# Kernel tuning notes

Measured on AMD Instinct MI355X. Metric: run time of the kernel, lower is better.

## Reference

```python
import jax, jax.numpy as jnp
import numpy as np
from jax import lax

N_SAMPLES = 2 ** 15      # 32768
D_SIZE = 256             # number of dictionary atoms
KERNEL = 256             # atom length
N_STEPS = 16             # sparse_coding_iterations
CHANNELS = 128


def setup_inputs() -> dict:
    key = jax.random.key(0)
    ks = jax.random.split(key, 9)
    B = 8
    x = jax.random.normal(ks[0], (B, N_SAMPLES), dtype=jnp.float32)
    # dictionary, initialized uniform(-1, 1) as in nn.Parameter(...).uniform_(-1, 1)
    d = jax.random.uniform(ks[1], (D_SIZE, KERNEL), dtype=jnp.float32, minval=-1.0, maxval=1.0)
    # 1x1 Conv1d weights stored as (out, in); biases (out,)
    w_pos_amp = jax.random.normal(ks[2], (CHANNELS, 2), dtype=jnp.float32) * 0.1
    b_pos_amp = jnp.zeros((CHANNELS,), dtype=jnp.float32)
    w_atoms = jax.random.normal(ks[3], (CHANNELS, D_SIZE), dtype=jnp.float32) * 0.05
    b_atoms = jnp.zeros((CHANNELS,), dtype=jnp.float32)
    w_reduce = jax.random.normal(ks[4], (CHANNELS, 2 * CHANNELS), dtype=jnp.float32) * 0.05
    b_reduce = jnp.zeros((CHANNELS,), dtype=jnp.float32)
    return {
        'x': x, 'd': d,
        'w_pos_amp': w_pos_amp, 'b_pos_amp': b_pos_amp,
        'w_atoms': w_atoms, 'b_atoms': b_atoms,
        'w_reduce': w_reduce, 'b_reduce': b_reduce,
    }


def _correlate(residual, d):
    # residual: (B, 1, N), d: (D, K) -> feature map (B, D, N-K+1) (valid cross-correlation,
    # identical to torch F.conv1d with no padding)
    return lax.conv_general_dilated(
        residual, d[:, None, :], window_strides=(1,), padding='VALID',
        dimension_numbers=('NCH', 'OIH', 'NCH'))


def _matching_pursuit(x3, d):
    """16-step greedy matching pursuit. Returns key points (B, 2+D, N_STEPS) and residual."""
    B = x3.shape[0]
    T = N_SAMPLES - KERNEL + 1  # valid correlation length

    def step(residual, _):
        fm = _correlate(residual, d)                       # (B, D, T)
        flat = fm.reshape(B, -1)
        idx = jnp.argmax(jnp.abs(flat), axis=1)            # best (atom, pos) per example
        amp = jnp.take_along_axis(flat, idx[:, None], axis=1)[:, 0]
        atom_idx = idx // T
        pos = idx % T

        def subtract(r, p, ai, a):
            seg = lax.dynamic_slice(r, (p,), (KERNEL,))
            return lax.dynamic_update_slice(r, seg - a * d[ai], (p,))

        new_res = jax.vmap(subtract)(residual[:, 0, :], pos, atom_idx, amp)[:, None, :]
        enc = jnp.concatenate([
            (pos.astype(jnp.float32) / T)[:, None],        # normalized position
            amp[:, None],                                  # amplitude
            jax.nn.one_hot(atom_idx, D_SIZE, dtype=jnp.float32),  # atom one-hot
        ], axis=1)                                         # (B, 2+D)
        return new_res, enc

    residual, encs = lax.scan(step, x3, None, length=N_STEPS)  # encs: (S, B, 2+D)
    kp = jnp.transpose(encs, (1, 2, 0))                        # (B, 2+D, S)
    return kp, residual


def _conv1x1(w, b, x):
    # w: (O, C), x: (B, C, T) -> (B, O, T)
    return jnp.einsum('oc,bct->bot', w, x) + b[None, :, None]


def reference(x, d, w_pos_amp, b_pos_amp, w_atoms, b_atoms, w_reduce, b_reduce):
    B = x.shape[0]
    x3 = x.reshape(B, 1, N_SAMPLES)
    kp, _ = _matching_pursuit(x3, d)          # (B, 258, 16)
    pos_amp = kp[:, :2, :]
    atoms = kp[:, 2:, :]
    pa = _conv1x1(w_pos_amp, b_pos_amp, pos_amp)
    at = _conv1x1(w_atoms, b_atoms, atoms)
    h = jnp.concatenate([pa, at], axis=1)     # (B, 2*channels, 16)
    return _conv1x1(w_reduce, b_reduce, h)    # (B, channels, 16)
```

## Files before the change

### kernel.cpp

```cpp
#include <hip/hip_runtime.h>
#include <hip/hip_bf16.h>
#include <float.h>

#define NS 32768
#define KER 256
#define TOUT 32513
#define NATOM 256
#define NSTEP 16
#define BATCH 8
#define NBLK 255
#define XSTR 33024
#define SW4(i) ((i) + (((i) >> 5) << 2))

typedef __attribute__((ext_vector_type(8))) _Float16 half8;
typedef __attribute__((ext_vector_type(16))) float f32x16;
typedef __attribute__((ext_vector_type(4))) unsigned int uint4v;

__device__ __forceinline__ void cmax(float& ba, float& bs, float& bi,
                                     float oa, float os, float oi) {
    if (oa > ba || (oa == ba && oi < bi)) { ba = oa; bs = os; bi = oi; }
}

__device__ __forceinline__ void fma8(float acc[8], float4 dA, float4 dB,
                                     float4 w0, float4 w1, float4 w2, float4 w3) {
    float w[16] = {w0.x,w0.y,w0.z,w0.w, w1.x,w1.y,w1.z,w1.w,
                   w2.x,w2.y,w2.z,w2.w, w3.x,w3.y,w3.z,w3.w};
    float dv[8] = {dA.x,dA.y,dA.z,dA.w, dB.x,dB.y,dB.z,dB.w};
#pragma unroll
    for (int i = 0; i < 8; ++i)
#pragma unroll
        for (int j = 0; j < 8; ++j)
            acc[j] = fmaf(dv[i], w[i + j], acc[j]);
}

__device__ __forceinline__ unsigned short f16hi(float v) {
    return __builtin_bit_cast(unsigned short, (_Float16)v);
}
__device__ __forceinline__ unsigned short f16lo(float v) {
    const _Float16 h = (_Float16)v;
    return __builtin_bit_cast(unsigned short, (_Float16)(v - (float)h));
}

__global__ __launch_bounds__(256) void k_prep(const float* __restrict__ x,
                                              const float* __restrict__ d,
                                              uint4* __restrict__ xhl4,
                                              uint4* __restrict__ dhF,
                                              uint4* __restrict__ dlF) {
    const int gid = blockIdx.x * 256 + threadIdx.x;
    const int NXE = BATCH * XSTR;
    if (gid < NXE) {
        const int b = gid / XSTR, i = gid - b * XSTR;
        float v[4];
#pragma unroll
        for (int u = 0; u < 4; ++u)
            v[u] = (i + u < NS) ? x[b * NS + i + u] : 0.f;
        uint4 q;
        q.x = (unsigned int)f16hi(v[0]) | ((unsigned int)f16hi(v[1]) << 16);
        q.y = (unsigned int)f16hi(v[2]) | ((unsigned int)f16hi(v[3]) << 16);
        q.z = (unsigned int)f16lo(v[0]) | ((unsigned int)f16lo(v[1]) << 16);
        q.w = (unsigned int)f16lo(v[2]) | ((unsigned int)f16lo(v[3]) << 16);
        xhl4[gid] = q;
    } else {
        const int j = gid - NXE;
        if (j < NATOM * 32) {
            const int kg = j >> 8, atom = j & 255;
            const float* dp = d + atom * 256 + (kg << 3);
            uint4 hw, lw;
            hw.x = (unsigned int)f16hi(dp[0]) | ((unsigned int)f16hi(dp[1]) << 16);
            hw.y = (unsigned int)f16hi(dp[2]) | ((unsigned int)f16hi(dp[3]) << 16);
            hw.z = (unsigned int)f16hi(dp[4]) | ((unsigned int)f16hi(dp[5]) << 16);
            hw.w = (unsigned int)f16hi(dp[6]) | ((unsigned int)f16hi(dp[7]) << 16);
            lw.x = (unsigned int)f16lo(dp[0]) | ((unsigned int)f16lo(dp[1]) << 16);
            lw.y = (unsigned int)f16lo(dp[2]) | ((unsigned int)f16lo(dp[3]) << 16);
            lw.z = (unsigned int)f16lo(dp[4]) | ((unsigned int)f16lo(dp[5]) << 16);
            lw.w = (unsigned int)f16lo(dp[6]) | ((unsigned int)f16lo(dp[7]) << 16);
            dhF[(kg << 8) + atom] = hw;
            dlF[(kg << 8) + atom] = lw;
        }
    }
}

__global__ __launch_bounds__(256) void k_init(const uint4* __restrict__ xhl4,
                                              const uint4* __restrict__ dhF,
                                              const uint4* __restrict__ dlF,
                                              float2* __restrict__ bm) {
    const int c = blockIdx.x, mg = blockIdx.y, b = blockIdx.z;
    const int tid = threadIdx.x;
    const int w = tid >> 6, l = tid & 63;
    const int n = l & 31, h = l >> 5;
    __shared__ uint4 xw[512];
    __shared__ unsigned long long wmax[4][64];
    const int t0 = c << 8;
    xw[tid] = xhl4[b * XSTR + t0 + tid];
    xw[tid + 256] = xhl4[b * XSTR + t0 + 256 + tid];
    __syncthreads();

    f32x16 acc00, acc01, acc10, acc11;
#pragma unroll
    for (int j = 0; j < 16; ++j) { acc00[j] = 0.f; acc01[j] = 0.f;
                                   acc10[j] = 0.f; acc11[j] = 0.f; }

    const int abase = (mg << 6) + n;
    const int sbb = (w << 6) + n + (h << 3);

    half8 fbh[4], fbl[4];
    {
        const uint4 q0 = xw[sbb], q1 = xw[sbb + 4];
        const uint4v hv = {q0.x, q0.y, q1.x, q1.y};
        const uint4v lv = {q0.z, q0.w, q1.z, q1.w};
        fbh[0] = __builtin_bit_cast(half8, hv);
        fbl[0] = __builtin_bit_cast(half8, lv);
    }
    {
        const uint4 q0 = xw[sbb + 16], q1 = xw[sbb + 20];
        const uint4v hv = {q0.x, q0.y, q1.x, q1.y};
        const uint4v lv = {q0.z, q0.w, q1.z, q1.w};
        fbh[1] = __builtin_bit_cast(half8, hv);
        fbl[1] = __builtin_bit_cast(half8, lv);
    }

#pragma unroll 4
    for (int kk = 0; kk < 16; ++kk) {
        const int kg = (kk << 1) + h;
        const half8 ah0 = __builtin_bit_cast(half8, dhF[(kg << 8) + abase]);
        const half8 al0 = __builtin_bit_cast(half8, dlF[(kg << 8) + abase]);
        const half8 ah1 = __builtin_bit_cast(half8, dhF[(kg << 8) + abase + 32]);
        const half8 al1 = __builtin_bit_cast(half8, dlF[(kg << 8) + abase + 32]);
        {
            const int sN = sbb + ((kk + 2) << 4);
            const uint4 q0 = xw[sN], q1 = xw[sN + 4];
            const uint4v hv = {q0.x, q0.y, q1.x, q1.y};
            const uint4v lv = {q0.z, q0.w, q1.z, q1.w};
            fbh[(kk + 2) & 3] = __builtin_bit_cast(half8, hv);
            fbl[(kk + 2) & 3] = __builtin_bit_cast(half8, lv);
        }
        const half8 b0h = fbh[kk & 3],       b0l = fbl[kk & 3];
        const half8 b1h = fbh[(kk + 2) & 3], b1l = fbl[(kk + 2) & 3];
        acc00 = __builtin_amdgcn_mfma_f32_32x32x16_f16(ah0, b0l, acc00, 0, 0, 0);
        acc00 = __builtin_amdgcn_mfma_f32_32x32x16_f16(al0, b0h, acc00, 0, 0, 0);
        acc00 = __builtin_amdgcn_mfma_f32_32x32x16_f16(ah0, b0h, acc00, 0, 0, 0);
        acc10 = __builtin_amdgcn_mfma_f32_32x32x16_f16(ah1, b0l, acc10, 0, 0, 0);
        acc10 = __builtin_amdgcn_mfma_f32_32x32x16_f16(al1, b0h, acc10, 0, 0, 0);
        acc10 = __builtin_amdgcn_mfma_f32_32x32x16_f16(ah1, b0h, acc10, 0, 0, 0);
        acc01 = __builtin_amdgcn_mfma_f32_32x32x16_f16(ah0, b1l, acc01, 0, 0, 0);
        acc01 = __builtin_amdgcn_mfma_f32_32x32x16_f16(al0, b1h, acc01, 0, 0, 0);
        acc01 = __builtin_amdgcn_mfma_f32_32x32x16_f16(ah0, b1h, acc01, 0, 0, 0);
        acc11 = __builtin_amdgcn_mfma_f32_32x32x16_f16(ah1, b1l, acc11, 0, 0, 0);
        acc11 = __builtin_amdgcn_mfma_f32_32x32x16_f16(al1, b1h, acc11, 0, 0, 0);
        acc11 = __builtin_amdgcn_mfma_f32_32x32x16_f16(ah1, b1h, acc11, 0, 0, 0);
    }

    const int tb = t0 + (w << 6) + n;
#pragma unroll
    for (int mt = 0; mt < 2; ++mt) {
#pragma unroll
        for (int r = 0; r < 16; ++r) {
            const int amt = (mt << 5) + (r & 3) + ((r >> 2) << 3) + (h << 2);
            const int idx0 = ((mg << 6) + amt) * TOUT + tb;
            const float v0 = (mt == 0) ? acc00[r] : acc10[r];
            const float v1 = (mt == 0) ? acc01[r] : acc11[r];
            const unsigned int c0 = (0x7FFFFFu - (unsigned int)idx0);
            unsigned long long k0 = 0ull, k1 = 0ull;
            if (tb < TOUT)
                k0 = ((unsigned long long)__float_as_uint(fabsf(v0)) << 32)
                   | ((unsigned long long)(c0 << 1))
                   | (unsigned long long)(__float_as_uint(v0) >> 31);
            if (tb + 32 < TOUT)
                k1 = ((unsigned long long)__float_as_uint(fabsf(v1)) << 32)
                   | ((unsigned long long)((c0 - 32u) << 1))
                   | (unsigned long long)(__float_as_uint(v1) >> 31);
            unsigned long long k = (k1 > k0) ? k1 : k0;
#pragma unroll
            for (int m = 1; m <= 16; m <<= 1) {
                const unsigned long long ok = __shfl_xor(k, m, 32);
                if (ok > k) k = ok;
            }
            if (n == 0) wmax[w][amt] = k;
        }
    }
    __syncthreads();
    if (tid < 128) {
        const int a = tid & 63, p = tid >> 6;
        unsigned long long k = wmax[(p << 1)][a];
        const unsigned long long k2 = wmax[(p << 1) + 1][a];
        if (k2 > k) k = k2;
        const int blk = (c << 1) + p;
        if (blk < NBLK) {
            const float av = __uint_as_float((unsigned int)(k >> 32));
            const unsigned int lo = (unsigned int)k;
            const int idx = 0x7FFFFF - (int)((lo >> 1) & 0x7FFFFFu);
            const float bsg = (lo & 1u) ? -av : av;
            bm[(size_t)((b << 8) + (mg << 6) + a) * NBLK + blk] =
                make_float2(bsg, (float)idx);
        }
    }
}

__global__ __launch_bounds__(256) void k_lvl2(const float2* __restrict__ bm,
                                              float4* __restrict__ l2) {
    const int b = blockIdx.y;
    const int oglob = blockIdx.x * 8 + (threadIdx.x >> 5);
    const int lane = threadIdx.x & 31;
    const float2* row = bm + (size_t)(b * NATOM + oglob) * NBLK;
    float ba = -1.f, bsg = 0.f, bi = 3.0e7f;
    for (int i = lane; i < NBLK; i += 32) {
        const float2 e = row[i];
        cmax(ba, bsg, bi, fabsf(e.x), e.x, e.y);
    }
#pragma unroll
    for (int m = 16; m >= 1; m >>= 1) {
        const float oa = __shfl_xor(ba, m, 32);
        const float os = __shfl_xor(bsg, m, 32);
        const float oi = __shfl_xor(bi, m, 32);
        cmax(ba, bsg, bi, oa, os, oi);
    }
    if (lane == 0) l2[(b << 8) + oglob] = make_float4(ba, bsg, bi, 0.f);
}

__global__ __launch_bounds__(512) void k_step(const float* __restrict__ d,
                                              const float* __restrict__ resid_src,
                                              float* __restrict__ resid_dst,
                                              float2* __restrict__ bm,
                                              float4* __restrict__ l2,
                                              int* __restrict__ pos_a,
                                              int* __restrict__ atom_a,
                                              float* __restrict__ amp_a,
                                              int step) {
    const int og = blockIdx.x, b = blockIdx.y;
    const int tid = threadIdx.x;
    const int wave = tid >> 6, lane = tid & 63;
    __shared__ float dt[2048];
    __shared__ float rsu[1024];
    __shared__ float4 sred[8];
    __shared__ float4 upd[8][5];
    __shared__ int sh_pos, sh_atom, sh_prev;
    __shared__ float sh_amp;

    ((float4*)dt)[tid] = ((const float4*)(d + og * 2048))[tid];
    if (tid == 0 && step >= 2) sh_prev = pos_a[(step - 1) * BATCH + b];
    const float4* l2r = l2 + (step & 1) * (BATCH * NATOM);
    float4*       l2w = l2 + ((step + 1) & 1) * (BATCH * NATOM);

    {
        float ba = -1.f, bsg = 0.f, bi = 3.0e7f;
        if (tid < 256) {
            const float4 e = l2r[(b << 8) + tid];
            ba = e.x; bsg = e.y; bi = e.z;
        }
#pragma unroll
        for (int m = 32; m >= 1; m >>= 1) {
            const float oa = __shfl_xor(ba, m);
            const float os = __shfl_xor(bsg, m);
            const float oi = __shfl_xor(bi, m);
            cmax(ba, bsg, bi, oa, os, oi);
        }
        if (lane == 0) sred[wave] = make_float4(ba, bsg, bi, 0.f);
    }
    __syncthreads();
    if (tid == 0) {
        float4 r = sred[0];
#pragma unroll
        for (int i = 1; i < 8; ++i) {
            const float4 q = sred[i];
            if (q.x > r.x || (q.x == r.x && q.z < r.z)) r = q;
        }
        const int idx = (int)r.z;
        const int atom = idx / TOUT;
        const int pos = idx - atom * TOUT;
        sh_pos = pos; sh_atom = atom; sh_amp = r.y;
        if (og == 0) {
            pos_a[step * BATCH + b] = pos;
            atom_a[step * BATCH + b] = atom;
            amp_a[step * BATCH + b] = r.y;
        }
    }
    __syncthreads();
    const int p = sh_pos, atom_s = sh_atom;
    const float amp = sh_amp;

    if (step < 2) {
        for (int i = tid; i < 1024; i += 512) {
            const int g = (og << 10) + i;
            float v = resid_src[(size_t)b * NS + g];
            const int off = g - p;
            if (off >= 0 && off < KER)
                v = __fsub_rn(v, __fmul_rn(amp, d[atom_s * KER + off]));
            resid_dst[(size_t)b * NS + g] = v;
        }
    } else if (og == 0) {
        if (tid < 256) {
            const int g = p + tid;
            resid_dst[(size_t)b * NS + g] =
                __fsub_rn(resid_src[(size_t)b * NS + g],
                          __fmul_rn(amp, d[atom_s * KER + tid]));
        } else {
            const int g = sh_prev + (tid - 256);
            if (g < p || g > p + 255)
                resid_dst[(size_t)b * NS + g] = resid_src[(size_t)b * NS + g];
        }
    }

    int tlo = p - 255; if (tlo < 0) tlo = 0;
    int thi = p + 255; if (thi > TOUT - 1) thi = TOUT - 1;
    const int bs0 = tlo >> 7, be0 = thi >> 7;
    const int rbase = bs0 << 7;
    const int nblks = be0 - bs0 + 1;
    const int rlen = (nblks << 7) + 255;
    for (int i = tid; i < rlen; i += 512) {
        const int g = rbase + i;
        float v = (g < NS) ? resid_src[(size_t)b * NS + g] : 0.f;
        const int off = g - p;
        if (g < NS && off >= 0 && off < KER)
            v = __fsub_rn(v, __fmul_rn(amp, d[atom_s * KER + off]));
        rsu[SW4(i)] = v;
    }
    __syncthreads();

    const int lg = lane >> 4, l16 = lane & 15;
    const float* dp = dt + (wave << 8) + (lg << 6);
    const int atomg = (og << 3) + wave;
    for (int bb = 0; bb < nblks; ++bb) {
        const int blk = bs0 + bb;
        const int t0r = (bb << 7) + (l16 << 3) + (lg << 6);
        float acc[8];
#pragma unroll
        for (int j = 0; j < 8; ++j) acc[j] = 0.f;
        float4 A0 = *(const float4*)(rsu + SW4(t0r));
        float4 A1 = *(const float4*)(rsu + SW4(t0r + 4));
        float4 B0 = *(const float4*)(rsu + SW4(t0r + 8));
        float4 B1 = *(const float4*)(rsu + SW4(t0r + 12));
#pragma unroll
        for (int kk = 0; kk < 64; kk += 16) {
            const float4 d0 = *(const float4*)(dp + kk);
            const float4 d1 = *(const float4*)(dp + kk + 4);
            const float4 N0 = *(const float4*)(rsu + SW4(t0r + kk + 16));
            const float4 N1 = *(const float4*)(rsu + SW4(t0r + kk + 20));
            fma8(acc, d0, d1, A0, A1, B0, B1);
            const float4 d2 = *(const float4*)(dp + kk + 8);
            const float4 d3 = *(const float4*)(dp + kk + 12);
            const float4 M0 = *(const float4*)(rsu + SW4(t0r + kk + 24));
            const float4 M1 = *(const float4*)(rsu + SW4(t0r + kk + 28));
            fma8(acc, d2, d3, B0, B1, N0, N1);
            A0 = N0; A1 = N1; B0 = M0; B1 = M1;
        }
#pragma unroll
        for (int j = 0; j < 8; ++j) {
            acc[j] += __shfl_xor(acc[j], 16);
            acc[j] += __shfl_xor(acc[j], 32);
        }
        float ba = -1.f, bsg = 0.f, bi = 3.0e7f;
        const int tbp = rbase + (bb << 7) + (l16 << 3);
#pragma unroll
        for (int j = 0; j < 8; ++j) {
            const int t = tbp + j;
            const float av = fabsf(acc[j]);
            if (t < TOUT && av > ba) { ba = av; bsg = acc[j]; bi = (float)(atomg * TOUT + t); }
        }
#pragma unroll
        for (int m = 32; m >= 1; m >>= 1) {
            const float oa = __shfl_xor(ba, m);
            const float os = __shfl_xor(bsg, m);
            const float oi = __shfl_xor(bi, m);
            cmax(ba, bsg, bi, oa, os, oi);
        }
        if (lane == 0) {
            bm[(size_t)(b * NATOM + atomg) * NBLK + blk] = make_float2(bsg, bi);
            upd[wave][bb] = make_float4(ba, bsg, bi, 0.f);
        }
    }
    __syncthreads();

    {
        const float4 eo = l2r[(b << 8) + atomg];
        const int oblk = ((int)eo.z - atomg * TOUT) >> 7;
        if (oblk >= bs0 && oblk <= be0) {
            float ba = -1.f, bsg = 0.f, bi = 3.0e7f;
            const float2* row = bm + (size_t)(b * NATOM + atomg) * NBLK;
            for (int i = lane; i < NBLK; i += 64) {
                if (i >= bs0 && i <= be0) {
                    const float4 e2 = upd[wave][i - bs0];
                    cmax(ba, bsg, bi, e2.x, e2.y, e2.z);
                } else {
                    const float2 e2 = row[i];
                    cmax(ba, bsg, bi, fabsf(e2.x), e2.x, e2.y);
                }
            }
#pragma unroll
            for (int m = 32; m >= 1; m >>= 1) {
                const float oa = __shfl_xor(ba, m);
                const float os = __shfl_xor(bsg, m);
                const float oi = __shfl_xor(bi, m);
                cmax(ba, bsg, bi, oa, os, oi);
            }
            if (lane == 0) l2w[(b << 8) + atomg] = make_float4(ba, bsg, bi, 0.f);
        } else if (lane == 0) {
            float ba = eo.x, bsg = eo.y, bi = eo.z;
            for (int bb = 0; bb < nblks; ++bb) {
                const float4 e2 = upd[wave][bb];
                cmax(ba, bsg, bi, e2.x, e2.y, e2.z);
            }
            l2w[(b << 8) + atomg] = make_float4(ba, bsg, bi, 0.f);
        }
    }
}

__global__ __launch_bounds__(128) void k_head(const int* __restrict__ pos_a,
                                              const int* __restrict__ atom_a,
                                              const float* __restrict__ amp_a,
                                              const float4* __restrict__ l2,
                                              const float* __restrict__ wpa,
                                              const float* __restrict__ bpa,
                                              const float* __restrict__ wat,
                                              const float* __restrict__ bat,
                                              const float* __restrict__ wr,
                                              const float* __restrict__ br,
                                              float* __restrict__ out) {
    const int s = blockIdx.x, b = blockIdx.y;
    const int o = threadIdx.x;
    __shared__ float4 hred[2];
    __shared__ int sh_pos, sh_atom;
    __shared__ float sh_amp;
    int pos, atom; float amp;
    if (s == NSTEP - 1) {
        const float4* l2r = l2 + ((NSTEP - 1) & 1) * (BATCH * NATOM);
        float ba = -1.f, bsg = 0.f, bi = 3.0e7f;
        const float4 e0 = l2r[(b << 8) + o];
        const float4 e1 = l2r[(b << 8) + 128 + o];
        cmax(ba, bsg, bi, e0.x, e0.y, e0.z);
        cmax(ba, bsg, bi, e1.x, e1.y, e1.z);
#pragma unroll
        for (int m = 32; m >= 1; m >>= 1) {
            const float oa = __shfl_xor(ba, m);
            const float os = __shfl_xor(bsg, m);
            const float oi = __shfl_xor(bi, m);
            cmax(ba, bsg, bi, oa, os, oi);
        }
        if ((o & 63) == 0) hred[o >> 6] = make_float4(ba, bsg, bi, 0.f);
        __syncthreads();
        if (o == 0) {
            float4 r = hred[0];
            const float4 q = hred[1];
            if (q.x > r.x || (q.x == r.x && q.z < r.z)) r = q;
            const int idx = (int)r.z;
            sh_atom = idx / TOUT;
            sh_pos = idx - sh_atom * TOUT;
            sh_amp = r.y;
        }
        __syncthreads();
        pos = sh_pos; atom = sh_atom; amp = sh_amp;
    } else {
        pos  = pos_a[s * BATCH + b];
        atom = atom_a[s * BATCH + b];
        amp  = amp_a[s * BATCH + b];
    }
    const float posn = (float)pos / 32513.0f;
    float sum = br[o];
    for (int c = 0; c < 128; ++c) {
        const float pa = wpa[c * 2] * posn + wpa[c * 2 + 1] * amp + bpa[c];
        const float at = wat[c * 256 + atom] + bat[c];
        sum += wr[o * 256 + c] * pa + wr[o * 256 + 128 + c] * at;
    }
    out[(b * 128 + o) * NSTEP + s] = sum;
}

extern "C" void kernel_launch(void* const* d_in, const int* in_sizes, int n_in,
                              void* d_out, int out_size, void* d_ws, size_t ws_size,
                              hipStream_t stream) {
    const float* x   = (const float*)d_in[0];
    const float* d   = (const float*)d_in[1];
    const float* wpa = (const float*)d_in[2];
    const float* bpa = (const float*)d_in[3];
    const float* wat = (const float*)d_in[4];
    const float* bat = (const float*)d_in[5];
    const float* wr  = (const float*)d_in[6];
    const float* br  = (const float*)d_in[7];
    float* out = (float*)d_out;

    char* ws = (char*)d_ws;
    float2* bm     = (float2*)ws;
    float4* l2     = (float4*)(ws + 4177920);
    int*    pos_a  = (int*)(ws + 4243456);
    int*    atom_a = (int*)(ws + 4243968);
    float*  amp_a  = (float*)(ws + 4244480);
    uint4*  dhF    = (uint4*)(ws + 4244992);
    uint4*  dlF    = (uint4*)(ws + 4376064);
    uint4*  xhl4   = (uint4*)(ws + 4507136);
    float*  resid0 = (float*)(ws + 4507136);
    float*  resid1 = (float*)(ws + 5555712);

    const int prep_n = BATCH * XSTR + NATOM * 32;
    k_prep<<<(prep_n + 255) / 256, 256, 0, stream>>>(x, d, xhl4, dhF, dlF);
    k_init<<<dim3(128, 4, 8), 256, 0, stream>>>(xhl4, dhF, dlF, bm);
    k_lvl2<<<dim3(32, 8), 256, 0, stream>>>(bm, l2);
    for (int st = 0; st < NSTEP - 1; ++st) {
        const float* rs = (st == 0) ? x : ((st & 1) ? resid1 : resid0);
        float* rd = (st & 1) ? resid0 : resid1;
        k_step<<<dim3(32, 8), 512, 0, stream>>>(d, rs, rd, bm, l2,
                                                pos_a, atom_a, amp_a, st);
    }
    k_head<<<dim3(16, 8), 128, 0, stream>>>(pos_a, atom_a, amp_a, l2,
                                            wpa, bpa, wat, bat, wr, br, out);
}
```

Measured before the change: 406.2 us.

## Fuse level-2 reduction into init via 64-bit atomicMax keys; halve init atom tile

Drops the separate k_lvl2 kernel. k_init now atomically max-reduces packed 64-bit (abs value, index, sign) keys straight into a per-atom level-2 array, and the step and head kernels use the same packed-key comparison instead of float4 triplets. k_init's atom tile shrinks from 64 to 32 per block, doubling the grid and halving accumulator registers, which may help occupancy but re-reads the x tile twice as often. It also adds a memset launch and global atomics in exchange for removing one kernel launch and the bm re-read.

New measurement: 407.5 us. About the same (+0.3%).

```diff
diff --git a/kernel.cpp b/kernel.cpp
--- a/kernel.cpp
+++ b/kernel.cpp
@@ -15,10 +15,23 @@
 typedef __attribute__((ext_vector_type(8))) _Float16 half8;
 typedef __attribute__((ext_vector_type(16))) float f32x16;
 typedef __attribute__((ext_vector_type(4))) unsigned int uint4v;
+typedef unsigned long long u64;
 
 __device__ __forceinline__ void cmax(float& ba, float& bs, float& bi,
                                      float oa, float os, float oi) {
     if (oa > ba || (oa == ba && oi < bi)) { ba = oa; bs = os; bi = oi; }
+}
+
+__device__ __forceinline__ u64 packkey(float sig, int idx) {
+    return ((u64)__float_as_uint(fabsf(sig)) << 32)
+         | ((u64)((0x7FFFFFu - (unsigned int)idx) << 1))
+         | (u64)(__float_as_uint(sig) >> 31);
+}
+__device__ __forceinline__ void unpackkey(u64 k, float& sig, int& idx) {
+    const float av = __uint_as_float((unsigned int)(k >> 32));
+    const unsigned int lo = (unsigned int)k;
+    idx = 0x7FFFFF - (int)((lo >> 1) & 0x7FFFFFu);
+    sig = (lo & 1u) ? -av : av;
 }
 
 __device__ __forceinline__ void fma8(float acc[8], float4 dA, float4 dB,
@@ -83,24 +96,24 @@
 __global__ __launch_bounds__(256) void k_init(const uint4* __restrict__ xhl4,
                                               const uint4* __restrict__ dhF,
                                               const uint4* __restrict__ dlF,
-                                              float2* __restrict__ bm) {
+                                              float2* __restrict__ bm,
+                                              u64* __restrict__ l2k) {
     const int c = blockIdx.x, mg = blockIdx.y, b = blockIdx.z;
     const int tid = threadIdx.x;
     const int w = tid >> 6, l = tid & 63;
     const int n = l & 31, h = l >> 5;
     __shared__ uint4 xw[512];
-    __shared__ unsigned long long wmax[4][64];
+    __shared__ u64 wmax[4][32];
     const int t0 = c << 8;
     xw[tid] = xhl4[b * XSTR + t0 + tid];
     xw[tid + 256] = xhl4[b * XSTR + t0 + 256 + tid];
     __syncthreads();
 
-    f32x16 acc00, acc01, acc10, acc11;
-#pragma unroll
-    for (int j = 0; j < 16; ++j) { acc00[j] = 0.f; acc01[j] = 0.f;
-                                   acc10[j] = 0.f; acc11[j] = 0.f; }
-
-    const int abase = (mg << 6) + n;
+    f32x16 acc00, acc01;
+#pragma unroll
+    for (int j = 0; j < 16; ++j) { acc00[j] = 0.f; acc01[j] = 0.f; }
+
+    const int abase = (mg << 5) + n;
     const int sbb = (w << 6) + n + (h << 3);
 
     half8 fbh[4], fbl[4];
@@ -124,8 +137,6 @@
         const int kg = (kk << 1) + h;
         const half8 ah0 = __builtin_bit_cast(half8, dhF[(kg << 8) + abase]);
         const half8 al0 = __builtin_bit_cast(half8, dlF[(kg << 8) + abase]);
-        const half8 ah1 = __builtin_bit_cast(half8, dhF[(kg << 8) + abase + 32]);
-        const half8 al1 = __builtin_bit_cast(half8, dlF[(kg << 8) + abase + 32]);
         {
             const int sN = sbb + ((kk + 2) << 4);
             const uint4 q0 = xw[sN], q1 = xw[sN + 4];
@@ -139,89 +150,58 @@
         acc00 = __builtin_amdgcn_mfma_f32_32x32x16_f16(ah0, b0l, acc00, 0, 0, 0);
         acc00 = __builtin_amdgcn_mfma_f32_32x32x16_f16(al0, b0h, acc00, 0, 0, 0);
         acc00 = __builtin_amdgcn_mfma_f32_32x32x16_f16(ah0, b0h, acc00, 0, 0, 0);
-        acc10 = __builtin_amdgcn_mfma_f32_32x32x16_f16(ah1, b0l, acc10, 0, 0, 0);
-        acc10 = __builtin_amdgcn_mfma_f32_32x32x16_f16(al1, b0h, acc10, 0, 0, 0);
-        acc10 = __builtin_amdgcn_mfma_f32_32x32x16_f16(ah1, b0h, acc10, 0, 0, 0);
         acc01 = __builtin_amdgcn_mfma_f32_32x32x16_f16(ah0, b1l, acc01, 0, 0, 0);
         acc01 = __builtin_amdgcn_mfma_f32_32x32x16_f16(al0, b1h, acc01, 0, 0, 0);
         acc01 = __builtin_amdgcn_mfma_f32_32x32x16_f16(ah0, b1h, acc01, 0, 0, 0);
-        acc11 = __builtin_amdgcn_mfma_f32_32x32x16_f16(ah1, b1l, acc11, 0, 0, 0);
-        acc11 = __builtin_amdgcn_mfma_f32_32x32x16_f16(al1, b1h, acc11, 0, 0, 0);
-        acc11 = __builtin_amdgcn_mfma_f32_32x32x16_f16(ah1, b1h, acc11, 0, 0, 0);
     }
 
     const int tb = t0 + (w << 6) + n;
 #pragma unroll
-    for (int mt = 0; mt < 2; ++mt) {
-#pragma unroll
-        for (int r = 0; r < 16; ++r) {
-            const int amt = (mt << 5) + (r & 3) + ((r >> 2) << 3) + (h << 2);
-            const int idx0 = ((mg << 6) + amt) * TOUT + tb;
-            const float v0 = (mt == 0) ? acc00[r] : acc10[r];
-            const float v1 = (mt == 0) ? acc01[r] : acc11[r];
-            const unsigned int c0 = (0x7FFFFFu - (unsigned int)idx0);
-            unsigned long long k0 = 0ull, k1 = 0ull;
-            if (tb < TOUT)
-                k0 = ((unsigned long long)__float_as_uint(fabsf(v0)) << 32)
-                   | ((unsigned long long)(c0 << 1))
-                   | (unsigned long long)(__float_as_uint(v0) >> 31);
-            if (tb + 32 < TOUT)
-                k1 = ((unsigned long long)__float_as_uint(fabsf(v1)) << 32)
-                   | ((unsigned long long)((c0 - 32u) << 1))
-                   | (unsigned long long)(__float_as_uint(v1) >> 31);
-            unsigned long long k = (k1 > k0) ? k1 : k0;
-#pragma unroll
-            for (int m = 1; m <= 16; m <<= 1) {
-                const unsigned long long ok = __shfl_xor(k, m, 32);
-                if (ok > k) k = ok;
-            }
-            if (n == 0) wmax[w][amt] = k;
-        }
-    }
-    __syncthreads();
-    if (tid < 128) {
-        const int a = tid & 63, p = tid >> 6;
-        unsigned long long k = wmax[(p << 1)][a];
-        const unsigned long long k2 = wmax[(p << 1) + 1][a];
+    for (int r = 0; r < 16; ++r) {
+        const int amt = (r & 3) + ((r >> 2) << 3) + (h << 2);
+        const int idx0 = ((mg << 5) + amt) * TOUT + tb;
+        const float v0 = acc00[r], v1 = acc01[r];
+        const unsigned int c0 = (0x7FFFFFu - (unsigned int)idx0);
+        u64 k0 = 0ull, k1 = 0ull;
+        if (tb < TOUT)
+            k0 = ((u64)__float_as_uint(fabsf(v0)) << 32)
+               | ((u64)(c0 << 1))
+               | (u64)(__float_as_uint(v0) >> 31);
+        if (tb + 32 < TOUT)
+            k1 = ((u64)__float_as_uint(fabsf(v1)) << 32)
+               | ((u64)((c0 - 32u) << 1))
+               | (u64)(__float_as_uint(v1) >> 31);
+        u64 k = (k1 > k0) ? k1 : k0;
+#pragma unroll
+        for (int m = 1; m <= 16; m <<= 1) {
+            const u64 ok = __shfl_xor(k, m, 32);
+            if (ok > k) k = ok;
+        }
+        if (n == 0) wmax[w][amt] = k;
+    }
+    __syncthreads();
+    if (tid < 64) {
+        const int a = tid & 31, p = tid >> 5;
+        u64 k = wmax[(p << 1)][a];
+        const u64 k2 = wmax[(p << 1) + 1][a];
         if (k2 > k) k = k2;
         const int blk = (c << 1) + p;
+        const int atom = (mg << 5) + a;
         if (blk < NBLK) {
-            const float av = __uint_as_float((unsigned int)(k >> 32));
-            const unsigned int lo = (unsigned int)k;
-            const int idx = 0x7FFFFF - (int)((lo >> 1) & 0x7FFFFFu);
-            const float bsg = (lo & 1u) ? -av : av;
-            bm[(size_t)((b << 8) + (mg << 6) + a) * NBLK + blk] =
+            float bsg; int idx;
+            unpackkey(k, bsg, idx);
+            bm[(size_t)((b << 8) + atom) * NBLK + blk] =
                 make_float2(bsg, (float)idx);
-        }
-    }
-}
-
-__global__ __launch_bounds__(256) void k_lvl2(const float2* __restrict__ bm,
-                                              float4* __restrict__ l2) {
-    const int b = blockIdx.y;
-    const int oglob = blockIdx.x * 8 + (threadIdx.x >> 5);
-    const int lane = threadIdx.x & 31;
-    const float2* row = bm + (size_t)(b * NATOM + oglob) * NBLK;
-    float ba = -1.f, bsg = 0.f, bi = 3.0e7f;
-    for (int i = lane; i < NBLK; i += 32) {
-        const float2 e = row[i];
-        cmax(ba, bsg, bi, fabsf(e.x), e.x, e.y);
-    }
-#pragma unroll
-    for (int m = 16; m >= 1; m >>= 1) {
-        const float oa = __shfl_xor(ba, m, 32);
-        const float os = __shfl_xor(bsg, m, 32);
-        const float oi = __shfl_xor(bi, m, 32);
-        cmax(ba, bsg, bi, oa, os, oi);
-    }
-    if (lane == 0) l2[(b << 8) + oglob] = make_float4(ba, bsg, bi, 0.f);
+            atomicMax(&l2k[(b << 8) + atom], k);
+        }
+    }
 }
 
 __global__ __launch_bounds__(512) void k_step(const float* __restrict__ d,
                                               const float* __restrict__ resid_src,
                                               float* __restrict__ resid_dst,
                                               float2* __restrict__ bm,
-                                              float4* __restrict__ l2,
+                                              u64* __restrict__ l2,
                                               int* __restrict__ pos_a,
                                               int* __restrict__ atom_a,
                                               float* __restrict__ amp_a,
@@ -231,47 +211,40 @@
     const int wave = tid >> 6, lane = tid & 63;
     __shared__ float dt[2048];
     __shared__ float rsu[1024];
-    __shared__ float4 sred[8];
+    __shared__ u64 sred[8];
     __shared__ float4 upd[8][5];
     __shared__ int sh_pos, sh_atom, sh_prev;
     __shared__ float sh_amp;
 
     ((float4*)dt)[tid] = ((const float4*)(d + og * 2048))[tid];
     if (tid == 0 && step >= 2) sh_prev = pos_a[(step - 1) * BATCH + b];
-    const float4* l2r = l2 + (step & 1) * (BATCH * NATOM);
-    float4*       l2w = l2 + ((step + 1) & 1) * (BATCH * NATOM);
+    u64* l2r = l2 + (step & 1) * (BATCH * NATOM);
+    u64* l2w = l2 + ((step + 1) & 1) * (BATCH * NATOM);
 
     {
-        float ba = -1.f, bsg = 0.f, bi = 3.0e7f;
-        if (tid < 256) {
-            const float4 e = l2r[(b << 8) + tid];
-            ba = e.x; bsg = e.y; bi = e.z;
-        }
-#pragma unroll
-        for (int m = 32; m >= 1; m >>= 1) {
-            const float oa = __shfl_xor(ba, m);
-            const float os = __shfl_xor(bsg, m);
-            const float oi = __shfl_xor(bi, m);
-            cmax(ba, bsg, bi, oa, os, oi);
-        }
-        if (lane == 0) sred[wave] = make_float4(ba, bsg, bi, 0.f);
+        u64 k = 0ull;
+        if (tid < 256) k = l2r[(b << 8) + tid];
+#pragma unroll
+        for (int m = 1; m <= 32; m <<= 1) {
+            const u64 ok = __shfl_xor(k, m);
+            if (ok > k) k = ok;
+        }
+        if (lane == 0) sred[wave] = k;
     }
     __syncthreads();
     if (tid == 0) {
-        float4 r = sred[0];
-#pragma unroll
-        for (int i = 1; i < 8; ++i) {
-            const float4 q = sred[i];
-            if (q.x > r.x || (q.x == r.x && q.z < r.z)) r = q;
-        }
-        const int idx = (int)r.z;
+        u64 k = sred[0];
+#pragma unroll
+        for (int i = 1; i < 8; ++i) if (sred[i] > k) k = sred[i];
+        float sig; int idx;
+        unpackkey(k, sig, idx);
         const int atom = idx / TOUT;
         const int pos = idx - atom * TOUT;
-        sh_pos = pos; sh_atom = atom; sh_amp = r.y;
+        sh_pos = pos; sh_atom = atom; sh_amp = sig;
         if (og == 0) {
             pos_a[step * BATCH + b] = pos;
             atom_a[step * BATCH + b] = atom;
-            amp_a[step * BATCH + b] = r.y;
+            amp_a[step * BATCH + b] = sig;
         }
     }
     __syncthreads();
@@ -371,8 +344,10 @@
     __syncthreads();
 
     {
-        const float4 eo = l2r[(b << 8) + atomg];
-        const int oblk = ((int)eo.z - atomg * TOUT) >> 7;
+        const u64 ko = l2r[(b << 8) + atomg];
+        float eox; int eidx;
+        unpackkey(ko, eox, eidx);
+        const int oblk = (eidx - atomg * TOUT) >> 7;
         if (oblk >= bs0 && oblk <= be0) {
             float ba = -1.f, bsg = 0.f, bi = 3.0e7f;
             const float2* row = bm + (size_t)(b * NATOM + atomg) * NBLK;
@@ -392,14 +367,15 @@
                 const float oi = __shfl_xor(bi, m);
                 cmax(ba, bsg, bi, oa, os, oi);
             }
-            if (lane == 0) l2w[(b << 8) + atomg] = make_float4(ba, bsg, bi, 0.f);
+            if (lane == 0) l2w[(b << 8) + atomg] = packkey(bsg, (int)bi);
         } else if (lane == 0) {
-            float ba = eo.x, bsg = eo.y, bi = eo.z;
+            u64 k = ko;
             for (int bb = 0; bb < nblks; ++bb) {
                 const float4 e2 = upd[wave][bb];
-                cmax(ba, bsg, bi, e2.x, e2.y, e2.z);
+                const u64 ku = packkey(e2.y, (int)e2.z);
+                if (ku > k) k = ku;
             }
-            l2w[(b << 8) + atomg] = make_float4(ba, bsg, bi, 0.f);
+            l2w[(b << 8) + atomg] = k;
         }
     }
 }
@@ -407,7 +383,7 @@
 __global__ __launch_bounds__(128) void k_head(const int* __restrict__ pos_a,
                                               const int* __restrict__ atom_a,
                                               const float* __restrict__ amp_a,
-                                              const float4* __restrict__ l2,
+                                              const u64* __restrict__ l2,
                                               const float* __restrict__ wpa,
                                               const float* __restrict__ bpa,
                                               const float* __restrict__ wat,
@@ -417,34 +393,30 @@
                                               float* __restrict__ out) {
     const int s = blockIdx.x, b = blockIdx.y;
     const int o = threadIdx.x;
-    __shared__ float4 hred[2];
+    __shared__ u64 hred[2];
     __shared__ int sh_pos, sh_atom;
     __shared__ float sh_amp;
     int pos, atom; float amp;
     if (s == NSTEP - 1) {
-        const float4* l2r = l2 + ((NSTEP - 1) & 1) * (BATCH * NATOM);
-        float ba = -1.f, bsg = 0.f, bi = 3.0e7f;
-        const float4 e0 = l2r[(b << 8) + o];
-        const float4 e1 = l2r[(b << 8) + 128 + o];
-        cmax(ba, bsg, bi, e0.x, e0.y, e0.z);
-        cmax(ba, bsg, bi, e1.x, e1.y, e1.z);
-#pragma unroll
-        for (int m = 32; m >= 1; m >>= 1) {
-            const float oa = __shfl_xor(ba, m);
-            const float os = __shfl_xor(bsg, m);
-            const float oi = __shfl_xor(bi, m);
-            cmax(ba, bsg, bi, oa, os, oi);
-        }
-        if ((o & 63) == 0) hred[o >> 6] = make_float4(ba, bsg, bi, 0.f);
+        const u64* l2r = l2 + ((NSTEP - 1) & 1) * (BATCH * NATOM);
+        u64 k = l2r[(b << 8) + o];
+        const u64 k2 = l2r[(b << 8) + 128 + o];
+        if (k2 > k) k = k2;
+#pragma unroll
+        for (int m = 1; m <= 32; m <<= 1) {
+            const u64 ok = __shfl_xor(k, m);
+            if (ok > k) k = ok;
+        }
+        if ((o & 63) == 0) hred[o >> 6] = k;
         __syncthreads();
         if (o == 0) {
-            float4 r = hred[0];
-            const float4 q = hred[1];
-            if (q.x > r.x || (q.x == r.x && q.z < r.z)) r = q;
-            const int idx = (int)r.z;
+            u64 r = hred[0];
+            if (hred[1] > r) r = hred[1];
+            float sig; int idx;
+            unpackkey(r, sig, idx);
             sh_atom = idx / TOUT;
             sh_pos = idx - sh_atom * TOUT;
-            sh_amp = r.y;
+            sh_amp = sig;
         }
         __syncthreads();
         pos = sh_pos; atom = sh_atom; amp = sh_amp;
@@ -477,27 +449,27 @@
     float* out = (float*)d_out;
 
     char* ws = (char*)d_ws;
-    float2* bm     = (float2*)ws;
-    float4* l2     = (float4*)(ws + 4177920);
-    int*    pos_a  = (int*)(ws + 4243456);
-    int*    atom_a = (int*)(ws + 4243968);
-    float*  amp_a  = (float*)(ws + 4244480);
-    uint4*  dhF    = (uint4*)(ws + 4244992);
-    uint4*  dlF    = (uint4*)(ws + 4376064);
-    uint4*  xhl4   = (uint4*)(ws + 4507136);
-    float*  resid0 = (float*)(ws + 4507136);
-    float*  resid1 = (float*)(ws + 5555712);
-
+    float2* bm    = (float2*)ws;
+    u64*    l2k   = (u64*)(ws + 4177920);
+    int*    pos_a  = (int*)(ws + 4210688);
+    int*    atom_a = (int*)(ws + 4211200);
+    float*  amp_a  = (float*)(ws + 4211712);
+    uint4*  dhF    = (uint4*)(ws + 4212224);
+    uint4*  dlF    = (uint4*)(ws + 4343296);
+    uint4*  xhl4   = (uint4*)(ws + 4474368);
+    float*  resid0 = (float*)(ws + 4474368);
+    float*  resid1 = (float*)(ws + 5522944);
+
+    hipMemsetAsync(l2k, 0, 32768, stream);
     const int prep_n = BATCH * XSTR + NATOM * 32;
     k_prep<<<(prep_n + 255) / 256, 256, 0, stream>>>(x, d, xhl4, dhF, dlF);
-    k_init<<<dim3(128, 4, 8), 256, 0, stream>>>(xhl4, dhF, dlF, bm);
-    k_lvl2<<<dim3(32, 8), 256, 0, stream>>>(bm, l2);
+    k_init<<<dim3(128, 8, 8), 256, 0, stream>>>(xhl4, dhF, dlF, bm, l2k);
     for (int st = 0; st < NSTEP - 1; ++st) {
         const float* rs = (st == 0) ? x : ((st & 1) ? resid1 : resid0);
         float* rd = (st & 1) ? resid0 : resid1;
-        k_step<<<dim3(32, 8), 512, 0, stream>>>(d, rs, rd, bm, l2,
+        k_step<<<dim3(32, 8), 512, 0, stream>>>(d, rs, rd, bm, l2k,
                                                 pos_a, atom_a, amp_a, st);
     }
-    k_head<<<dim3(16, 8), 128, 0, stream>>>(pos_a, atom_a, amp_a, l2,
+    k_head<<<dim3(16, 8), 128, 0, stream>>>(pos_a, atom_a, amp_a, l2k,
                                             wpa, bpa, wat, bat, wr, br, out);
 }
```
